# Kernel tuning notes

Measured on AMD Instinct MI355X. Metric: run time of the kernel, lower is better.

Reference implementation:

```python
import jax, jax.numpy as jnp
import numpy as np

T1 = 4096
T2 = 4096
EMB = 512
W_BAND = 128  # sliding-window width w; band half-width = w//2


def band_mask(t2, t1, w, dtype=jnp.float32):
    # torch code fills diagonals -i..i for i in range(w//2) -> |col-row| < w//2
    r = jnp.arange(t2)[:, None]
    c = jnp.arange(t1)[None, :]
    return (jnp.abs(c - r) < (w // 2)).astype(dtype)


def setup_inputs() -> dict:
    key = jax.random.key(0)
    ks = jax.random.split(key, 7)
    return {
        "x1": jax.random.normal(ks[0], (T1, T1), dtype=jnp.float32),
        "x2": jax.random.normal(ks[1], (T1, T2), dtype=jnp.float32),
        "W1": jax.random.normal(ks[2], (EMB, T1), dtype=jnp.float32) * 0.02,
        "b1": jax.random.normal(ks[3], (EMB,), dtype=jnp.float32) * 0.02,
        "W2": jax.random.normal(ks[4], (EMB, T2), dtype=jnp.float32) * 0.02,
        "b2": jax.random.normal(ks[5], (EMB,), dtype=jnp.float32) * 0.02,
        "global_att": jax.random.normal(ks[6], (T2, T1), dtype=jnp.float32),
    }


def reference(x1, x2, W1, b1, W2, b2, global_att):
    # decoder branch: lin1: T1->emb applied to x1, lin2: T2->emb applied to x2
    h1 = x1 @ W1.T + b1                      # (T1, emb)
    h2 = x2 @ W2.T + b2                      # (T1, emb)
    dotted = h1 @ h2.T                       # (T1, T1)  == np.dot(x1, x2^T)
    mask = band_mask(T2, T1, W_BAND)         # (T2, T1) banded 0/1
    local_att = mask @ dotted                # (T2, T1) banded row-sum of dotted
    lg = local_att + global_att              # add dense 'global' term
    return jax.nn.softmax(lg, axis=0)        # softmax over dim 0, per original
```

## Files before the change

kernel.cpp:

```cpp
#include <hip/hip_runtime.h>

typedef unsigned short u16;
using f32x4  = __attribute__((ext_vector_type(4))) float;
using bf16x8 = __attribute__((ext_vector_type(8))) __bf16;

__device__ __forceinline__ u16 f2bf(float f) {
  unsigned u = __builtin_bit_cast(unsigned, f);
  u += 0x7FFFu + ((u >> 16) & 1u);
  return (u16)(u >> 16);
}
__device__ __forceinline__ float bf2f(u16 h) {
  unsigned u = ((unsigned)h) << 16;
  return __builtin_bit_cast(float, u);
}

__device__ __forceinline__ void split2(float f0, float f1, unsigned& hi, unsigned& lo) {
  unsigned u0 = __builtin_bit_cast(unsigned, f0);
  unsigned u1 = __builtin_bit_cast(unsigned, f1);
  unsigned r0 = u0 + (0x7FFFu + ((u0 >> 16) & 1u));
  unsigned r1 = u1 + (0x7FFFu + ((u1 >> 16) & 1u));
  hi = (r0 >> 16) | (r1 & 0xFFFF0000u);
  float h0 = __builtin_bit_cast(float, r0 & 0xFFFF0000u);
  float h1 = __builtin_bit_cast(float, r1 & 0xFFFF0000u);
  unsigned l0 = __builtin_bit_cast(unsigned, f0 - h0);
  unsigned l1 = __builtin_bit_cast(unsigned, f1 - h1);
  lo = (l0 >> 16) | (l1 & 0xFFFF0000u);
}

__device__ __forceinline__ void gload_lds16(const void* g, void* l) {
  __builtin_amdgcn_global_load_lds((__attribute__((address_space(1))) void*)g,
                                   (__attribute__((address_space(3))) void*)l,
                                   16, 0, 0);
}

__global__ __launch_bounds__(256) void split_kernel(
    const float* __restrict__ x, u16* __restrict__ hi, u16* __restrict__ lo, int n4)
{
  const size_t t = (size_t)blockIdx.x * 256 + threadIdx.x;
  if (t >= (size_t)n4) return;
  float4 v = ((const float4*)x)[t];
  uint2 hp, lp;
  split2(v.x, v.y, hp.x, lp.x);
  split2(v.z, v.w, hp.y, lp.y);
  ((uint2*)hi)[t] = hp;
  ((uint2*)lo)[t] = lp;
}

__global__ __launch_bounds__(256) void gemm1_k(
    const float* __restrict__ x1, const float* __restrict__ x2,
    const u16* __restrict__ WH, const u16* __restrict__ WL,
    const float* __restrict__ b1, const float* __restrict__ b2,
    float* __restrict__ hp0, float* __restrict__ hp1,
    float* __restrict__ hp2, float* __restrict__ hp3)
{
  constexpr int K = 4096, NC = 1024, KC = 1024, NT = KC / 32;
  __shared__ __align__(16) float lA[2][128 * 32];
  __shared__ __align__(16) u16 lBh[2][128 * 32];
  __shared__ __align__(16) u16 lBl[2][128 * 32];

  const int tid  = threadIdx.x;
  const int lane = tid & 63;
  const int wave = tid >> 6;
  const int quad = lane >> 4;
  const int l16  = lane & 15;

  const int m0    = blockIdx.x * 128;
  const int n0    = blockIdx.y * 128;
  const int batch = (n0 >= 512);
  const float* Ag   = batch ? x2 : x1;
  const float* bias = batch ? b2 : b1;
  const int z = blockIdx.z;
  float* hp = (z == 0) ? hp0 : (z == 1) ? hp1 : (z == 2) ? hp2 : hp3;
  const int k00 = z * KC;

  const int rA = tid >> 3, cA = tid & 7;
  const int rB = tid >> 2, cB = tid & 3;

  auto stage = [&](int buf, int kt) {
    const int ko = k00 + kt * 32;
#pragma unroll
    for (int t = 0; t < 4; ++t) {
      const int r  = t * 32 + rA;
      const int cs = (cA + r) & 7;
      gload_lds16(Ag + (size_t)(m0 + r) * K + ko + cs * 4,
                  (char*)lA[buf] + t * 4096 + tid * 16);
    }
#pragma unroll
    for (int t = 0; t < 2; ++t) {
      const int r  = t * 64 + rB;
      const int cs = (cB + (r >> 1)) & 3;
      gload_lds16(WH + (size_t)(n0 + r) * K + ko + cs * 8,
                  (char*)lBh[buf] + t * 4096 + tid * 16);
      gload_lds16(WL + (size_t)(n0 + r) * K + ko + cs * 8,
                  (char*)lBl[buf] + t * 4096 + tid * 16);
    }
  };

  f32x4 acc[2][8] = {};

  stage(0, 0);
  stage(1, 1);

  for (int kt = 0; kt < NT; ++kt) {
    const int cur = kt & 1;
    __builtin_amdgcn_sched_barrier(0);
    if (kt < NT - 1) asm volatile("s_waitcnt vmcnt(8)" ::: "memory");
    else             asm volatile("s_waitcnt vmcnt(0)" ::: "memory");
    __builtin_amdgcn_s_barrier();
    __builtin_amdgcn_sched_barrier(0);

    bf16x8 ah[2], al[2], bh[8], bl[8];
#pragma unroll
    for (int i = 0; i < 2; ++i) {
      const int R = wave * 32 + i * 16 + l16;
      const float4 f0 = *(const float4*)&lA[cur][R * 32 + ((2 * quad - R) & 7) * 4];
      const float4 f1 = *(const float4*)&lA[cur][R * 32 + ((2 * quad + 1 - R) & 7) * 4];
      uint4 h, l;
      split2(f0.x, f0.y, h.x, l.x); split2(f0.z, f0.w, h.y, l.y);
      split2(f1.x, f1.y, h.z, l.z); split2(f1.z, f1.w, h.w, l.w);
      ah[i] = __builtin_bit_cast(bf16x8, h);
      al[i] = __builtin_bit_cast(bf16x8, l);
    }
#pragma unroll
    for (int j = 0; j < 8; ++j) {
      const int R = j * 16 + l16;
      const int c = (quad - (R >> 1)) & 3;
      bh[j] = *(const bf16x8*)&lBh[cur][R * 32 + c * 8];
      bl[j] = *(const bf16x8*)&lBl[cur][R * 32 + c * 8];
    }
    __builtin_amdgcn_s_setprio(1);
#pragma unroll
    for (int i = 0; i < 2; ++i)
#pragma unroll
      for (int j = 0; j < 8; ++j) {
        acc[i][j] = __builtin_amdgcn_mfma_f32_16x16x32_bf16(ah[i], bh[j], acc[i][j], 0, 0, 0);
        acc[i][j] = __builtin_amdgcn_mfma_f32_16x16x32_bf16(ah[i], bl[j], acc[i][j], 0, 0, 0);
        acc[i][j] = __builtin_amdgcn_mfma_f32_16x16x32_bf16(al[i], bh[j], acc[i][j], 0, 0, 0);
      }
    __builtin_amdgcn_s_setprio(0);

    __builtin_amdgcn_sched_barrier(0);
    __builtin_amdgcn_s_barrier();
    __builtin_amdgcn_sched_barrier(0);
    if (kt + 2 < NT) stage(cur, kt + 2);
  }

#pragma unroll
  for (int i = 0; i < 2; ++i)
#pragma unroll
    for (int j = 0; j < 8; ++j) {
      const int gn = n0 + j * 16 + l16;
      const float bv = (z == 0) ? bias[gn - batch * 512] : 0.0f;
#pragma unroll
      for (int r = 0; r < 4; ++r) {
        const int gm = m0 + wave * 32 + i * 16 + quad * 4 + r;
        hp[(size_t)gm * NC + gn] = acc[i][j][r] + bv;
      }
    }
}

__global__ __launch_bounds__(256) void gemm2_k(
    const u16* __restrict__ AH, const u16* __restrict__ AL,
    const u16* __restrict__ BH, const u16* __restrict__ BL,
    const float* __restrict__ ga, float* __restrict__ C,
    float* __restrict__ pm, float* __restrict__ ps)
{
  constexpr int K = 512, N = 4096, NT = K / 32;
  __shared__ __align__(16) u16 lAh[2][128 * 32];
  __shared__ __align__(16) u16 lAl[2][128 * 32];
  __shared__ __align__(16) u16 lBh[2][128 * 32];
  __shared__ __align__(16) u16 lBl[2][128 * 32];

  const int tid  = threadIdx.x;
  const int lane = tid & 63;
  const int wave = tid >> 6;
  const int wr   = wave >> 1, wc = wave & 1;
  const int quad = lane >> 4;
  const int l16  = lane & 15;

  const int m0 = blockIdx.x * 128;
  const int n0 = blockIdx.y * 128;

  const int rB = tid >> 2, cB = tid & 3;

  auto stage = [&](int buf, int kt) {
    const int ko = kt * 32;
#pragma unroll
    for (int t = 0; t < 2; ++t) {
      const int r  = t * 64 + rB;
      const int cs = (cB + (r >> 1)) & 3;
      const size_t goA = (size_t)(m0 + r) * K + ko + cs * 8;
      const size_t goB = (size_t)(n0 + r) * K + ko + cs * 8;
      gload_lds16(AH + goA, (char*)lAh[buf] + t * 4096 + tid * 16);
      gload_lds16(AL + goA, (char*)lAl[buf] + t * 4096 + tid * 16);
      gload_lds16(BH + goB, (char*)lBh[buf] + t * 4096 + tid * 16);
      gload_lds16(BL + goB, (char*)lBl[buf] + t * 4096 + tid * 16);
    }
  };

  f32x4 acc[4][4] = {};

  stage(0, 0);
  stage(1, 1);

  for (int kt = 0; kt < NT; ++kt) {
    const int cur = kt & 1;
    __builtin_amdgcn_sched_barrier(0);
    if (kt < NT - 1) asm volatile("s_waitcnt vmcnt(8)" ::: "memory");
    else             asm volatile("s_waitcnt vmcnt(0)" ::: "memory");
    __builtin_amdgcn_s_barrier();
    __builtin_amdgcn_sched_barrier(0);

    bf16x8 ah[4], al[4], bh[4], bl[4];
#pragma unroll
    for (int i = 0; i < 4; ++i) {
      const int R = wr * 64 + i * 16 + l16;
      const int c = (quad - (R >> 1)) & 3;
      ah[i] = *(const bf16x8*)&lAh[cur][R * 32 + c * 8];
      al[i] = *(const bf16x8*)&lAl[cur][R * 32 + c * 8];
    }
#pragma unroll
    for (int j = 0; j < 4; ++j) {
      const int R = wc * 64 + j * 16 + l16;
      const int c = (quad - (R >> 1)) & 3;
      bh[j] = *(const bf16x8*)&lBh[cur][R * 32 + c * 8];
      bl[j] = *(const bf16x8*)&lBl[cur][R * 32 + c * 8];
    }
    __builtin_amdgcn_s_setprio(1);
#pragma unroll
    for (int i = 0; i < 4; ++i)
#pragma unroll
      for (int j = 0; j < 4; ++j) {
        acc[i][j] = __builtin_amdgcn_mfma_f32_16x16x32_bf16(ah[i], bh[j], acc[i][j], 0, 0, 0);
        acc[i][j] = __builtin_amdgcn_mfma_f32_16x16x32_bf16(ah[i], bl[j], acc[i][j], 0, 0, 0);
        acc[i][j] = __builtin_amdgcn_mfma_f32_16x16x32_bf16(al[i], bh[j], acc[i][j], 0, 0, 0);
      }
    __builtin_amdgcn_s_setprio(0);

    __builtin_amdgcn_sched_barrier(0);
    __builtin_amdgcn_s_barrier();
    __builtin_amdgcn_sched_barrier(0);
    if (kt + 2 < NT) stage(cur, kt + 2);
  }

#pragma unroll
  for (int i = 0; i < 4; ++i)
#pragma unroll
    for (int j = 0; j < 4; ++j) {
      const int gn = n0 + wc * 64 + j * 16 + l16;
#pragma unroll
      for (int r = 0; r < 4; ++r) {
        const int gm = m0 + wr * 64 + i * 16 + quad * 4 + r;
        const size_t idx = (size_t)gm * N + gn;
        const float v = acc[i][j][r] + ga[idx];
        C[idx] = v;
        acc[i][j][r] = v;
      }
    }

  float* red = (float*)lAh;
#pragma unroll
  for (int j = 0; j < 4; ++j) {
    float m = -3.0e38f;
#pragma unroll
    for (int i = 0; i < 4; ++i)
#pragma unroll
      for (int r = 0; r < 4; ++r) m = fmaxf(m, acc[i][j][r]);
    float s = 0.f;
#pragma unroll
    for (int i = 0; i < 4; ++i)
#pragma unroll
      for (int r = 0; r < 4; ++r) s += __expf(acc[i][j][r] - m);
#pragma unroll
    for (int off = 16; off <= 32; off <<= 1) {
      const float mo = __shfl_xor(m, off);
      const float so = __shfl_xor(s, off);
      const float mn = fmaxf(m, mo);
      s = s * __expf(m - mn) + so * __expf(mo - mn);
      m = mn;
    }
    if (quad == 0) {
      const int col = wc * 64 + j * 16 + l16;
      red[(wr * 128 + col) * 2 + 0] = m;
      red[(wr * 128 + col) * 2 + 1] = s;
    }
  }
  __syncthreads();
  if (tid < 128) {
    const float ma = red[(0 * 128 + tid) * 2 + 0], sa = red[(0 * 128 + tid) * 2 + 1];
    const float mb = red[(1 * 128 + tid) * 2 + 0], sb = red[(1 * 128 + tid) * 2 + 1];
    const float mm = fmaxf(ma, mb);
    const float ss = sa * __expf(ma - mm) + sb * __expf(mb - mm);
    pm[(size_t)blockIdx.x * N + n0 + tid] = mm;
    ps[(size_t)blockIdx.x * N + n0 + tid] = ss;
  }
}

__global__ __launch_bounds__(256) void bandsum_kernel(
    const float* __restrict__ hp0, const float* __restrict__ hp1,
    const float* __restrict__ hp2, const float* __restrict__ hp3,
    u16* __restrict__ sh, u16* __restrict__ sl, int M)
{
  const int c = blockIdx.y * 256 + threadIdx.x;
  const int R = blockIdx.x * 64;
  float s = 0.f;
  for (int k = R - 63; k < R + 63; ++k)
    if (k >= 0 && k < M) {
      const size_t o = (size_t)k * 1024 + c;
      s += (hp0[o] + hp1[o]) + (hp2[o] + hp3[o]);
    }
  for (int i = R; i < R + 64; ++i) {
    const int ka = i + 63;
    if (ka < M) {
      const size_t o = (size_t)ka * 1024 + c;
      s += (hp0[o] + hp1[o]) + (hp2[o] + hp3[o]);
    }
    const u16 hb = f2bf(s);
    sh[(size_t)i * 512 + c] = hb;
    sl[(size_t)i * 512 + c] = f2bf(s - bf2f(hb));
    const int kr = i - 63;
    if (kr >= 0) {
      const size_t o = (size_t)kr * 1024 + c;
      s -= (hp0[o] + hp1[o]) + (hp2[o] + hp3[o]);
    }
  }
}

__global__ __launch_bounds__(256) void h2split_kernel(
    const float* __restrict__ hp0, const float* __restrict__ hp1,
    const float* __restrict__ hp2, const float* __restrict__ hp3,
    u16* __restrict__ hh, u16* __restrict__ hl)
{
  const size_t t = (size_t)blockIdx.x * 256 + threadIdx.x;
  const size_t row = t >> 7;
  const int c4 = (int)(t & 127) * 4;
  const size_t o = row * 1024 + 512 + c4;
  const float4 a = *(const float4*)&hp0[o];
  const float4 b = *(const float4*)&hp1[o];
  const float4 d = *(const float4*)&hp2[o];
  const float4 e = *(const float4*)&hp3[o];
  uint2 hp, lp;
  split2((a.x + b.x) + (d.x + e.x), (a.y + b.y) + (d.y + e.y), hp.x, lp.x);
  split2((a.z + b.z) + (d.z + e.z), (a.w + b.w) + (d.w + e.w), hp.y, lp.y);
  *(uint2*)&hh[row * 512 + c4] = hp;
  *(uint2*)&hl[row * 512 + c4] = lp;
}

__global__ __launch_bounds__(256) void colcombine_kernel(
    const float* __restrict__ pm, const float* __restrict__ ps,
    float* __restrict__ cv, int N, int nb)
{
  const int j = blockIdx.x * 256 + threadIdx.x;
  float m = -3.0e38f;
  for (int b = 0; b < nb; ++b) m = fmaxf(m, pm[(size_t)b * N + j]);
  float s = 0.f;
  for (int b = 0; b < nb; ++b) s += ps[(size_t)b * N + j] * __expf(pm[(size_t)b * N + j] - m);
  cv[j] = m + __logf(s);
}

__global__ __launch_bounds__(256) void norm_kernel(
    float* __restrict__ lg, const float* __restrict__ cv, int N)
{
  const size_t t = (size_t)blockIdx.x * 256 + threadIdx.x;
  float4 v = ((const float4*)lg)[t];
  const int j4 = (int)(t % (size_t)(N / 4));
  const float4 c = ((const float4*)cv)[j4];
  float4 o;
  o.x = __expf(v.x - c.x);
  o.y = __expf(v.y - c.y);
  o.z = __expf(v.z - c.z);
  o.w = __expf(v.w - c.w);
  ((float4*)lg)[t] = o;
}

extern "C" void kernel_launch(void* const* d_in, const int* in_sizes, int n_in,
                              void* d_out, int out_size, void* d_ws, size_t ws_size,
                              hipStream_t stream)
{
  const float* x1 = (const float*)d_in[0];
  const float* x2 = (const float*)d_in[1];
  const float* W1 = (const float*)d_in[2];
  const float* b1 = (const float*)d_in[3];
  const float* W2 = (const float*)d_in[4];
  const float* b2 = (const float*)d_in[5];
  const float* ga = (const float*)d_in[6];
  float* out = (float*)d_out;

  const int T = 4096, E = 512;

  float* hp0 = out;
  float* hp1 = out + (size_t)T * 1024;
  float* hp2 = out + (size_t)T * 2048;
  float* hp3 = out + (size_t)T * 3072;

  char* w = (char*)d_ws;
  u16* WH  = (u16*)w;  w += (size_t)2 * E * T * 2;
  u16* WL  = (u16*)w;  w += (size_t)2 * E * T * 2;
  u16* S1H = (u16*)w;  w += (size_t)T * E * 2;
  u16* S1L = (u16*)w;  w += (size_t)T * E * 2;
  u16* H2H = (u16*)w;  w += (size_t)T * E * 2;
  u16* H2L = (u16*)w;  w += (size_t)T * E * 2;
  float* pm = (float*)w; w += (size_t)32 * T * 4;
  float* ps = (float*)w; w += (size_t)32 * T * 4;
  float* cv = (float*)w; w += (size_t)T * 4;

  split_kernel<<<E * T / 1024, 256, 0, stream>>>(W1, WH, WL, E * T / 4);
  split_kernel<<<E * T / 1024, 256, 0, stream>>>(
      W2, WH + (size_t)E * T, WL + (size_t)E * T, E * T / 4);

  gemm1_k<<<dim3(T / 128, 8, 4), 256, 0, stream>>>(
      x1, x2, WH, WL, b1, b2, hp0, hp1, hp2, hp3);

  bandsum_kernel<<<dim3(T / 64, 2), 256, 0, stream>>>(
      hp0, hp1, hp2, hp3, S1H, S1L, T);
  h2split_kernel<<<T * (E / 4) / 256, 256, 0, stream>>>(
      hp0, hp1, hp2, hp3, H2H, H2L);

  gemm2_k<<<dim3(T / 128, T / 128), 256, 0, stream>>>(
      S1H, S1L, H2H, H2L, ga, out, pm, ps);

  colcombine_kernel<<<T / 256, 256, 0, stream>>>(pm, ps, cv, T, 32);
  norm_kernel<<<T * T / 1024, 256, 0, stream>>>(out, cv, T);
}
```

Measured before the change: 488.4 us.

## Use packed bf16 convert for split, prefetch global_att, shrink bandsum rows

Swaps the software round-to-nearest bf16 hi/lo split in gemm1 for the hardware v_cvt_pk_bf16_f32 instruction, which cuts ALU work in the MFMA inner loop. In gemm2, the global_att tile is loaded into registers at the start of the last K iteration, so its latency overlaps the final MFMAs instead of stalling the epilogue. The bandsum kernel now handles 16 rows per block instead of 64, giving more blocks and more parallelism. The cost is more redundant window-priming reads and extra register pressure from the 64 prefetched floats.

```diff
diff --git a/kernel.cpp b/kernel.cpp
--- a/kernel.cpp
+++ b/kernel.cpp
@@ -27,6 +27,16 @@
   lo = (l0 >> 16) | (l1 & 0xFFFF0000u);
 }
 
+__device__ __forceinline__ void split2_pk(float f0, float f1, unsigned& hi, unsigned& lo) {
+  unsigned h;
+  asm("v_cvt_pk_bf16_f32 %0, %1, %2" : "=v"(h) : "v"(f0), "v"(f1));
+  const float h0 = __builtin_bit_cast(float, h << 16);
+  const float h1 = __builtin_bit_cast(float, h & 0xFFFF0000u);
+  unsigned l;
+  asm("v_cvt_pk_bf16_f32 %0, %1, %2" : "=v"(l) : "v"(f0 - h0), "v"(f1 - h1));
+  hi = h; lo = l;
+}
+
 __device__ __forceinline__ void gload_lds16(const void* g, void* l) {
   __builtin_amdgcn_global_load_lds((__attribute__((address_space(1))) void*)g,
                                    (__attribute__((address_space(3))) void*)l,
@@ -116,8 +126,8 @@
       const float4 f0 = *(const float4*)&lA[cur][R * 32 + ((2 * quad - R) & 7) * 4];
       const float4 f1 = *(const float4*)&lA[cur][R * 32 + ((2 * quad + 1 - R) & 7) * 4];
       uint4 h, l;
-      split2(f0.x, f0.y, h.x, l.x); split2(f0.z, f0.w, h.y, l.y);
-      split2(f1.x, f1.y, h.z, l.z); split2(f1.z, f1.w, h.w, l.w);
+      split2_pk(f0.x, f0.y, h.x, l.x); split2_pk(f0.z, f0.w, h.y, l.y);
+      split2_pk(f1.x, f1.y, h.z, l.z); split2_pk(f1.z, f1.w, h.w, l.w);
       ah[i] = __builtin_bit_cast(bf16x8, h);
       al[i] = __builtin_bit_cast(bf16x8, l);
     }
@@ -199,6 +209,7 @@
   };
 
   f32x4 acc[4][4] = {};
+  float ga_r[4][4][4];
 
   stage(0, 0);
   stage(1, 1);
@@ -210,6 +221,20 @@
     else             asm volatile("s_waitcnt vmcnt(0)" ::: "memory");
     __builtin_amdgcn_s_barrier();
     __builtin_amdgcn_sched_barrier(0);
+
+    if (kt == NT - 1) {
+#pragma unroll
+      for (int i = 0; i < 4; ++i)
+#pragma unroll
+        for (int j = 0; j < 4; ++j) {
+          const int gn = n0 + wc * 64 + j * 16 + l16;
+#pragma unroll
+          for (int r = 0; r < 4; ++r) {
+            const int gm = m0 + wr * 64 + i * 16 + quad * 4 + r;
+            ga_r[i][j][r] = ga[(size_t)gm * N + gn];
+          }
+        }
+    }
 
     bf16x8 ah[4], al[4], bh[4], bl[4];
 #pragma unroll
@@ -252,7 +277,7 @@
       for (int r = 0; r < 4; ++r) {
         const int gm = m0 + wr * 64 + i * 16 + quad * 4 + r;
         const size_t idx = (size_t)gm * N + gn;
-        const float v = acc[i][j][r] + ga[idx];
+        const float v = acc[i][j][r] + ga_r[i][j][r];
         C[idx] = v;
         acc[i][j][r] = v;
       }
@@ -301,15 +326,16 @@
     const float* __restrict__ hp2, const float* __restrict__ hp3,
     u16* __restrict__ sh, u16* __restrict__ sl, int M)
 {
+  constexpr int ROWS = 16;
   const int c = blockIdx.y * 256 + threadIdx.x;
-  const int R = blockIdx.x * 64;
+  const int R = blockIdx.x * ROWS;
   float s = 0.f;
   for (int k = R - 63; k < R + 63; ++k)
     if (k >= 0 && k < M) {
       const size_t o = (size_t)k * 1024 + c;
       s += (hp0[o] + hp1[o]) + (hp2[o] + hp3[o]);
     }
-  for (int i = R; i < R + 64; ++i) {
+  for (int i = R; i < R + ROWS; ++i) {
     const int ka = i + 63;
     if (ka < M) {
       const size_t o = (size_t)ka * 1024 + c;
@@ -411,7 +437,7 @@
   gemm1_k<<<dim3(T / 128, 8, 4), 256, 0, stream>>>(
       x1, x2, WH, WL, b1, b2, hp0, hp1, hp2, hp3);
 
-  bandsum_kernel<<<dim3(T / 64, 2), 256, 0, stream>>>(
+  bandsum_kernel<<<dim3(T / 16, 2), 256, 0, stream>>>(
       hp0, hp1, hp2, hp3, S1H, S1L, T);
   h2split_kernel<<<T * (E / 4) / 256, 256, 0, stream>>>(
       hp0, hp1, hp2, hp3, H2H, H2L);
```

Measured after the change: 460.3 us. -5.8%, faster.
